# Kernel tuning notes

Hardware: AMD Instinct MI355X
Metric: run time of the kernel (lower is better)

The kernel has to match this reference:

```python
import jax, jax.numpy as jnp
import numpy as np

N = 50000
E = 1600000
D_IN = 128
D_OUT = 128


def setup_inputs() -> dict:
    key = jax.random.key(0)
    k1, k2, k3, k4 = jax.random.split(key, 4)
    x = jax.random.normal(k1, (N, D_IN), dtype=jnp.float32)
    edge_index = jax.random.randint(k2, (2, E), 0, N, dtype=jnp.int64)
    # Linear(in_channels, out_channels) params (torch layout: W [out, in])
    bound = 1.0 / np.sqrt(D_IN)
    W = jax.random.uniform(k3, (D_OUT, D_IN), minval=-bound, maxval=bound, dtype=jnp.float32)
    b = jax.random.uniform(k4, (D_OUT,), minval=-bound, maxval=bound, dtype=jnp.float32)
    return {"x": x, "edge_index": edge_index, "W": W, "b": b}


def reference(x, edge_index, W, b):
    src, dst = edge_index[0], edge_index[1]
    # degree of each node as a source: tg.utils.degree(edge_index[0])
    deg = jax.ops.segment_sum(jnp.ones((E,), dtype=x.dtype), src, num_segments=N)
    norm = jnp.sqrt(deg + 1.0)[:, None]  # [N, 1]
    xn = x / norm
    # message passing with self_loop=True: scatter-add into x itself (out=x)
    agg = xn + jax.ops.segment_sum(xn[src], dst, num_segments=N)  # [N, D_IN]
    h = agg / norm
    return h @ W.T + b
```

## Files before the change

### kernel.cpp

```cpp
#include <hip/hip_runtime.h>

#define NN 50000
#define NE 1600000
#define D 128
#define RPB 40
#define NR 2
#define RNG 25000
#define NC 32
#define CHUNK 50000
#define NC2 64
#define CHUNK2 25000
#define NB 49

#define WS_INV  0
#define WS_CNT  204800
#define WS_OFF  409600
#define WS_BSUM 610304
#define WS_WT   614400
#define WS_PDST 679936
#define WS_PSRC 13479936
#define WS_CSR  16679936
#define WS_XNB  679936

__global__ __launch_bounds__(1024) void fused_pre(const int* __restrict__ ei,
                                                  const float* __restrict__ W,
                                                  unsigned short* __restrict__ psrc,
                                                  int* __restrict__ pdst,
                                                  float* __restrict__ Wt) {
    __shared__ int h[RNG];
    int bid = blockIdx.x;
    if (bid < 64) {
        int r = bid >> 5, c = bid & 31;
        int lo = r * RNG;
        for (int j = threadIdx.x; j < RNG; j += 1024) h[j] = 0;
        __syncthreads();
        const int* s = ei + c * CHUNK;
        for (int i = threadIdx.x; i < CHUNK; i += 1024) {
            int k = s[i] - lo;
            if ((unsigned)k < RNG) atomicAdd(&h[k], 1);
        }
        __syncthreads();
        unsigned short* p = psrc + (size_t)bid * RNG;
        for (int j = threadIdx.x; j < RNG; j += 1024) p[j] = (unsigned short)h[j];
    } else if (bid < 192) {
        int b2 = bid - 64;
        int r = b2 >> 6, c = b2 & 63;
        int lo = r * RNG;
        for (int j = threadIdx.x; j < RNG; j += 1024) h[j] = 0;
        __syncthreads();
        const int* d = ei + NE + c * CHUNK2;
        for (int i = threadIdx.x; i < CHUNK2; i += 1024) {
            int k = d[i] - lo;
            if ((unsigned)k < RNG) atomicAdd(&h[k], 1);
        }
        __syncthreads();
        int* p = pdst + (size_t)b2 * RNG;
        for (int j = threadIdx.x; j < RNG; j += 1024) p[j] = h[j];
    } else {
        int i = (bid - 192) * 1024 + threadIdx.x;
        int c = i >> 7, k = i & 127;
        Wt[k * D + c] = W[i];
    }
}

__global__ void reduce_both(const unsigned short* __restrict__ psrc,
                            const int* __restrict__ pdst,
                            float* __restrict__ inv, int* __restrict__ cnt) {
    int k = blockIdx.x * blockDim.x + threadIdx.x;
    if (k >= NN) return;
    int r = k / RNG, j = k - r * RNG;
    size_t bs = (size_t)(r * NC) * RNG + j;
    int s = 0;
#pragma unroll 8
    for (int c = 0; c < NC; ++c) s += psrc[bs + (size_t)c * RNG];
    size_t bd = (size_t)(r * NC2) * RNG + j;
    int t = 0;
#pragma unroll 8
    for (int c = 0; c < NC2; ++c) t += pdst[bd + (size_t)c * RNG];
    inv[k] = rsqrtf((float)s + 1.0f);
    cnt[k] = t;
}

__global__ __launch_bounds__(1024) void scan_blocks(const int* __restrict__ cnt,
                                                    int* __restrict__ off,
                                                    int* __restrict__ bsum) {
    __shared__ int s[1024];
    int tid = threadIdx.x;
    int i = blockIdx.x * 1024 + tid;
    int v = (i < NN) ? cnt[i] : 0;
    s[tid] = v;
    __syncthreads();
    for (int d = 1; d < 1024; d <<= 1) {
        int t = (tid >= d) ? s[tid - d] : 0;
        __syncthreads();
        s[tid] += t;
        __syncthreads();
    }
    if (i < NN) off[i] = s[tid] - v;
    if (tid == 1023) bsum[blockIdx.x] = s[1023];
}

__global__ void scan_chunks(int* __restrict__ pdst, int* __restrict__ off,
                            const int* __restrict__ bsum) {
    int k = blockIdx.x * blockDim.x + threadIdx.x;
    if (k >= NN) return;
    int bi = k >> 10;
    int top = 0;
#pragma unroll 8
    for (int c = 0; c < bi; ++c) top += bsum[c];
    int run = off[k] + top;
    off[k] = run;
    int r = k / RNG, j = k - r * RNG;
    size_t base = (size_t)(r * NC2) * RNG + j;
#pragma unroll 8
    for (int c = 0; c < NC2; ++c) {
        size_t p = base + (size_t)c * RNG;
        int v = pdst[p];
        pdst[p] = run;
        run += v;
    }
}

__global__ __launch_bounds__(1024) void fill_sorted(const int* __restrict__ ei,
                                                    const int* __restrict__ bases,
                                                    unsigned short* __restrict__ csr) {
    __shared__ int cur[RNG];
    int r = blockIdx.x >> 6, c = blockIdx.x & 63;
    int lo = r * RNG;
    const int* bslice = bases + (size_t)blockIdx.x * RNG;
    for (int j = threadIdx.x; j < RNG; j += 1024) cur[j] = bslice[j];
    __syncthreads();
    const int* s = ei + c * CHUNK2;
    const int* d = ei + NE + c * CHUNK2;
    for (int i = threadIdx.x; i < CHUNK2; i += 1024) {
        int kd = d[i] - lo;
        if ((unsigned)kd < RNG) {
            int pos = atomicAdd(&cur[kd], 1);
            csr[pos] = (unsigned short)s[i];
        }
    }
}

__device__ __forceinline__ unsigned bf16_rne(float f) {
    unsigned u = __float_as_uint(f);
    return (u + 0x7fffu + ((u >> 16) & 1u)) >> 16;
}
__global__ void scale_kernel(const float* __restrict__ x, const float* __restrict__ inv,
                             unsigned* __restrict__ xnb4) {
    int i = blockIdx.x * blockDim.x + threadIdx.x;
    if (i >= NN * 16) return;
    int row = i >> 4;
    float w = inv[row];
    const float4* src = (const float4*)(x + (size_t)i * 8);
    float4 a = src[0], bq = src[1];
    uint4 o;
    o.x = bf16_rne(a.x * w)  | (bf16_rne(a.y * w) << 16);
    o.y = bf16_rne(a.z * w)  | (bf16_rne(a.w * w) << 16);
    o.z = bf16_rne(bq.x * w) | (bf16_rne(bq.y * w) << 16);
    o.w = bf16_rne(bq.z * w) | (bf16_rne(bq.w * w) << 16);
    ((uint4*)xnb4)[i] = o;
}

__global__ __launch_bounds__(256) void gather_kernel(const unsigned* __restrict__ xnb,
                                                     const float* __restrict__ inv,
                                                     const int* __restrict__ off,
                                                     const int* __restrict__ cnt,
                                                     const unsigned short* __restrict__ csr,
                                                     float* __restrict__ out) {
    int wid = (blockIdx.x * blockDim.x + threadIdx.x) >> 6;
    if (wid >= NN) return;
    int lane = threadIdx.x & 63;
    int half = lane >> 5;
    int col4 = lane & 31;

    float ax = 0.f, ay = 0.f, az = 0.f, aw = 0.f;
    const uint2* xb = (const uint2*)xnb;
    if (half == 0) {
        uint2 u = xb[(size_t)wid * 32 + col4];
        ax = __uint_as_float(u.x << 16);
        ay = __uint_as_float(u.x & 0xffff0000u);
        az = __uint_as_float(u.y << 16);
        aw = __uint_as_float(u.y & 0xffff0000u);
    }
    int n = cnt[wid];
    const unsigned short* row = csr + off[wid];
    int i = half;
    for (; i + 6 < n; i += 8) {
        int s0 = row[i], s1 = row[i + 2], s2 = row[i + 4], s3 = row[i + 6];
        uint2 u0 = xb[(size_t)s0 * 32 + col4];
        uint2 u1 = xb[(size_t)s1 * 32 + col4];
        uint2 u2 = xb[(size_t)s2 * 32 + col4];
        uint2 u3 = xb[(size_t)s3 * 32 + col4];
        ax += __uint_as_float(u0.x << 16) + __uint_as_float(u1.x << 16)
            + __uint_as_float(u2.x << 16) + __uint_as_float(u3.x << 16);
        ay += __uint_as_float(u0.x & 0xffff0000u) + __uint_as_float(u1.x & 0xffff0000u)
            + __uint_as_float(u2.x & 0xffff0000u) + __uint_as_float(u3.x & 0xffff0000u);
        az += __uint_as_float(u0.y << 16) + __uint_as_float(u1.y << 16)
            + __uint_as_float(u2.y << 16) + __uint_as_float(u3.y << 16);
        aw += __uint_as_float(u0.y & 0xffff0000u) + __uint_as_float(u1.y & 0xffff0000u)
            + __uint_as_float(u2.y & 0xffff0000u) + __uint_as_float(u3.y & 0xffff0000u);
    }
    for (; i < n; i += 2) {
        int s = row[i];
        uint2 u = xb[(size_t)s * 32 + col4];
        ax += __uint_as_float(u.x << 16);
        ay += __uint_as_float(u.x & 0xffff0000u);
        az += __uint_as_float(u.y << 16);
        aw += __uint_as_float(u.y & 0xffff0000u);
    }
    ax += __shfl_xor(ax, 32, 64);
    ay += __shfl_xor(ay, 32, 64);
    az += __shfl_xor(az, 32, 64);
    aw += __shfl_xor(aw, 32, 64);
    if (half == 0) {
        float wn = inv[wid];
        float4 o;
        o.x = ax * wn; o.y = ay * wn; o.z = az * wn; o.w = aw * wn;
        ((float4*)(out + (size_t)wid * D))[col4] = o;
    }
}

__global__ __launch_bounds__(256) void gemm_kernel(float* io, const float* __restrict__ Wt,
                                                   const float* __restrict__ b) {
    __shared__ float h[RPB][D];
    int r0 = blockIdx.x * RPB;

    const float4* src4 = (const float4*)(io + (size_t)r0 * D);
    for (int t = threadIdx.x; t < RPB * D / 4; t += 256) {
        ((float4*)h)[t] = src4[t];
    }
    __syncthreads();

    int c = threadIdx.x & 127;
    int rh = threadIdx.x >> 7;
    float acc[20];
#pragma unroll
    for (int j = 0; j < 20; ++j) acc[j] = 0.0f;

    for (int k0 = 0; k0 < D; k0 += 4) {
        float w0 = Wt[(k0 + 0) * D + c];
        float w1 = Wt[(k0 + 1) * D + c];
        float w2 = Wt[(k0 + 2) * D + c];
        float w3 = Wt[(k0 + 3) * D + c];
#pragma unroll
        for (int j = 0; j < 20; ++j) {
            float4 hv = *(const float4*)&h[rh * 20 + j][k0];
            acc[j] += hv.x * w0 + hv.y * w1 + hv.z * w2 + hv.w * w3;
        }
    }

    float bc = b[c];
#pragma unroll
    for (int j = 0; j < 20; ++j) {
        io[(size_t)(r0 + rh * 20 + j) * D + c] = acc[j] + bc;
    }
}

extern "C" void kernel_launch(void* const* d_in, const int* in_sizes, int n_in,
                              void* d_out, int out_size, void* d_ws, size_t ws_size,
                              hipStream_t stream) {
    const float* x  = (const float*)d_in[0];
    const int*   ei = (const int*)d_in[1];
    const float* W  = (const float*)d_in[2];
    const float* b  = (const float*)d_in[3];
    float* out = (float*)d_out;

    char* ws = (char*)d_ws;
    float*          inv  = (float*)         (ws + WS_INV);
    int*            cnt  = (int*)           (ws + WS_CNT);
    int*            off  = (int*)           (ws + WS_OFF);
    int*            bsum = (int*)           (ws + WS_BSUM);
    float*          Wt   = (float*)         (ws + WS_WT);
    int*            pdst = (int*)           (ws + WS_PDST);
    unsigned short* psrc = (unsigned short*)(ws + WS_PSRC);
    unsigned short* csr  = (unsigned short*)(ws + WS_CSR);
    unsigned*       xnb  = (unsigned*)      (ws + WS_XNB);

    fused_pre<<<208, 1024, 0, stream>>>(ei, W, psrc, pdst, Wt);
    reduce_both<<<(NN + 255) / 256, 256, 0, stream>>>(psrc, pdst, inv, cnt);
    scan_blocks<<<NB, 1024, 0, stream>>>(cnt, off, bsum);
    scan_chunks<<<(NN + 255) / 256, 256, 0, stream>>>(pdst, off, bsum);
    fill_sorted<<<NR * NC2, 1024, 0, stream>>>(ei, pdst, csr);
    scale_kernel<<<(NN * 16 + 255) / 256, 256, 0, stream>>>(x, inv, xnb);
    gather_kernel<<<(NN * 64 + 255) / 256, 256, 0, stream>>>(xnb, inv, off, cnt, csr, out);
    gemm_kernel<<<NN / RPB, 256, 0, stream>>>(out, Wt, b);
}
```

Measured before the change: 169.1 us.

## Fuse neighbor gather and linear projection into one kernel via LDS

Merges the gather kernel and the GEMM kernel. Each 1024-thread block gathers 16 destination rows, one wave per row, writes them into shared memory, then applies the 128x128 weight matrix and bias directly. This removes the round trip of the aggregated fp32 intermediate through global memory and one kernel launch. In exchange each thread now computes only 2 output rows, so W is re-read far more often per row, and the block barrier makes all 16 rows wait for the slowest wave's gather.

```diff
diff --git a/kernel.cpp b/kernel.cpp
--- a/kernel.cpp
+++ b/kernel.cpp
@@ -3,7 +3,7 @@
 #define NN 50000
 #define NE 1600000
 #define D 128
-#define RPB 40
+#define RPB 16
 #define NR 2
 #define RNG 25000
 #define NC 32
@@ -161,15 +161,20 @@
     ((uint4*)xnb4)[i] = o;
 }
 
-__global__ __launch_bounds__(256) void gather_kernel(const unsigned* __restrict__ xnb,
-                                                     const float* __restrict__ inv,
-                                                     const int* __restrict__ off,
-                                                     const int* __restrict__ cnt,
-                                                     const unsigned short* __restrict__ csr,
-                                                     float* __restrict__ out) {
-    int wid = (blockIdx.x * blockDim.x + threadIdx.x) >> 6;
-    if (wid >= NN) return;
-    int lane = threadIdx.x & 63;
+__global__ __launch_bounds__(1024) void gather_gemm(const unsigned* __restrict__ xnb,
+                                                    const float* __restrict__ inv,
+                                                    const int* __restrict__ off,
+                                                    const int* __restrict__ cnt,
+                                                    const unsigned short* __restrict__ csr,
+                                                    const float* __restrict__ Wt,
+                                                    const float* __restrict__ b,
+                                                    float* __restrict__ out) {
+    __shared__ float h[RPB][D];
+    int r0 = blockIdx.x * RPB;
+    int tid = threadIdx.x;
+    int widx = tid >> 6;
+    int wid = r0 + widx;
+    int lane = tid & 63;
     int half = lane >> 5;
     int col4 = lane & 31;
 
@@ -216,44 +221,28 @@
         float wn = inv[wid];
         float4 o;
         o.x = ax * wn; o.y = ay * wn; o.z = az * wn; o.w = aw * wn;
-        ((float4*)(out + (size_t)wid * D))[col4] = o;
-    }
-}
-
-__global__ __launch_bounds__(256) void gemm_kernel(float* io, const float* __restrict__ Wt,
-                                                   const float* __restrict__ b) {
-    __shared__ float h[RPB][D];
-    int r0 = blockIdx.x * RPB;
-
-    const float4* src4 = (const float4*)(io + (size_t)r0 * D);
-    for (int t = threadIdx.x; t < RPB * D / 4; t += 256) {
-        ((float4*)h)[t] = src4[t];
+        *(float4*)&h[widx][col4 * 4] = o;
     }
     __syncthreads();
 
-    int c = threadIdx.x & 127;
-    int rh = threadIdx.x >> 7;
-    float acc[20];
-#pragma unroll
-    for (int j = 0; j < 20; ++j) acc[j] = 0.0f;
-
+    int c = tid & 127;
+    int g = tid >> 7;
+    float acc0 = 0.f, acc1 = 0.f;
+    const float* hr0 = h[g * 2];
+    const float* hr1 = h[g * 2 + 1];
     for (int k0 = 0; k0 < D; k0 += 4) {
         float w0 = Wt[(k0 + 0) * D + c];
         float w1 = Wt[(k0 + 1) * D + c];
         float w2 = Wt[(k0 + 2) * D + c];
         float w3 = Wt[(k0 + 3) * D + c];
-#pragma unroll
-        for (int j = 0; j < 20; ++j) {
-            float4 hv = *(const float4*)&h[rh * 20 + j][k0];
-            acc[j] += hv.x * w0 + hv.y * w1 + hv.z * w2 + hv.w * w3;
-        }
-    }
-
+        float4 h0 = *(const float4*)&hr0[k0];
+        float4 h1 = *(const float4*)&hr1[k0];
+        acc0 += h0.x * w0 + h0.y * w1 + h0.z * w2 + h0.w * w3;
+        acc1 += h1.x * w0 + h1.y * w1 + h1.z * w2 + h1.w * w3;
+    }
     float bc = b[c];
-#pragma unroll
-    for (int j = 0; j < 20; ++j) {
-        io[(size_t)(r0 + rh * 20 + j) * D + c] = acc[j] + bc;
-    }
+    out[(size_t)(r0 + g * 2) * D + c]     = acc0 + bc;
+    out[(size_t)(r0 + g * 2 + 1) * D + c] = acc1 + bc;
 }
 
 extern "C" void kernel_launch(void* const* d_in, const int* in_sizes, int n_in,
@@ -282,6 +271,5 @@
     scan_chunks<<<(NN + 255) / 256, 256, 0, stream>>>(pdst, off, bsum);
     fill_sorted<<<NR * NC2, 1024, 0, stream>>>(ei, pdst, csr);
     scale_kernel<<<(NN * 16 + 255) / 256, 256, 0, stream>>>(x, inv, xnb);
-    gather_kernel<<<(NN * 64 + 255) / 256, 256, 0, stream>>>(xnb, inv, off, cnt, csr, out);
-    gemm_kernel<<<NN / RPB, 256, 0, stream>>>(out, Wt, b);
-}
+    gather_gemm<<<NN / RPB, 1024, 0, stream>>>(xnb, inv, off, cnt, csr, Wt, b, out);
+}
```

Measured after the change: 178.2 us. +5.3%, slower.
